# Performance work log

Hardware: AMD Instinct MI355X
Metric: run time of the kernel (lower is better)

## Reference

```python
import jax, jax.numpy as jnp
import numpy as np

N = 20000   # nodes
E = 320000  # edges
C = 64      # channel multiplicity
NB = 8      # bessel basis size
NA = 4      # node attribute (species) dim
L_DIMS = (1, 3, 5)  # 2l+1 for l=0,1,2
SH = 9      # total spherical-harmonic dim
OFFS = (0, 1, 4, 9)


def setup_inputs() -> dict:
    key = jax.random.key(0)
    ks = jax.random.split(key, 11)
    s = lambda k, shape: jax.random.normal(k, shape, dtype=jnp.float32)
    return {
        "length": jax.random.uniform(ks[0], (E, NB), dtype=jnp.float32),
        "node_features": s(ks[1], (N, C)),
        "node_attributes": s(ks[2], (N, NA)),
        "edge_attributes": s(ks[3], (E, SH)),
        "W1": s(ks[4], (NB, 64)),
        "W2": s(ks[5], (64, 64)),
        "W3": s(ks[6], (64, 64)),
        "W4": s(ks[7], (64, 3 * C)),
        "Wl": s(ks[8], (3, C, C)),
        "Wsc": s(ks[9], (NA, C, C)),
        "edge_index": jax.random.randint(ks[10], (2, E), 0, N, dtype=jnp.int32),
    }


def reference(length, node_features, node_attributes, edge_attributes, W1, W2, W3, W4, Wl, Wsc, edge_index):
    sender, receiver = edge_index[0], edge_index[1]
    silu = jax.nn.silu
    # e3nn FullyConnectedNet: x @ W / sqrt(fan_in), silu between layers, no act on last
    h = silu(length @ W1 * np.float32(1.0 / np.sqrt(NB)))
    h = silu(h @ W2 * np.float32(0.125))
    h = silu(h @ W3 * np.float32(0.125))
    w = (h @ W4 * np.float32(0.125)).reshape(E, 3, C)  # per-edge TP weights [E,3,C]
    # weighted tensor product: scalar node feats x sh (0e x le -> le, uvu)
    wx = w * node_features[sender][:, None, :]          # [E,3,C]
    parts = []
    for l in range(3):
        Y = edge_attributes[:, OFFS[l]:OFFS[l + 1]]     # [E, 2l+1]
        parts.append((wx[:, l, :, None] * Y[:, None, :]).reshape(E, C * L_DIMS[l]))
    mij = jnp.concatenate(parts, axis=1)                # [E, C*9]
    # scatter_sum into receivers
    msg = jax.ops.segment_sum(mij, receiver, num_segments=N)  # [N, C*9]
    # e3nn Linear: per-l channel mix, 1/sqrt(fan_in) norm
    out_blocks = []
    o = 0
    for l in range(3):
        d = L_DIMS[l]
        blk = msg[:, o:o + C * d].reshape(N, C, d)
        out_blocks.append(jnp.einsum('num,uv->nvm', blk, Wl[l]) * np.float32(1.0 / np.sqrt(C)))
        o += C * d
    message = jnp.concatenate(out_blocks, axis=2)       # reshape_irreps -> [N, C, 9]
    # FullyConnectedTensorProduct(attr 0e, feat 0e) -> only 0e output has paths
    sc0 = jnp.einsum('na,nu,auw->nw', node_attributes, node_features, Wsc) * np.float32(1.0 / np.sqrt(NA * C))
    sc = jnp.concatenate([sc0, jnp.zeros((N, C * (SH - 1)), dtype=sc0.dtype)], axis=1)  # [N, C*9]
    return (message, sc)
```

## Files before the change

kernel.cpp:

```cpp
#include <hip/hip_runtime.h>
#include <hip/hip_fp16.h>

#define N_NODES 20000
#define N_EDGES 320000
#define MSG_ROW 576
#define MSG_OFF 11520000
#define SCAN_BS 256
#define NBLK_SCAN ((N_NODES + SCAN_BS - 1) / SCAN_BS)
#define NPAD 20032
#define MT_S (NPAD * 64)

typedef _Float16 f16;
typedef _Float16 f16x4 __attribute__((ext_vector_type(4)));
typedef _Float16 f16x8 __attribute__((ext_vector_type(8)));
typedef float f32x4 __attribute__((ext_vector_type(4)));

#define OFF_WT4 0
#define OFF_W1T 24576
#define OFF_WT2 28672
#define OFF_WT3 36864
#define OFF_H0  45056
#define OFF_HT  49152
#define LDS_TOTAL 57344
#define OFF_WXT 24576

#define OFF_WLT  22528
#define OFF_WSCT 34816
#define WIMG_HALF 51200
#define WIMG_BYTES 102400

__device__ __forceinline__ float silu_f(float x) {
    return x * (1.0f / (1.0f + __expf(-x)));
}


__global__ __launch_bounds__(256)
void wimg_kernel(const float* __restrict__ W1, const float* __restrict__ W2,
                 const float* __restrict__ W3, const float* __restrict__ W4,
                 const float* __restrict__ Wl, const float* __restrict__ Wsc,
                 f16* __restrict__ img) {
    const int p = blockIdx.x * 256 + threadIdx.x;
    if (p >= WIMG_HALF) return;
    float v;
    if (p < 12288) {
        const int m = p >> 6, rem = p & 63, g = rem >> 3, j = rem & 7;
        const int k = ((g ^ (m & 7)) << 3) | j;
        v = W4[k * 192 + m];
    } else if (p < 14336) {
        const int q = p - 12288;
        const int m = q >> 5, rem = q & 31, g = rem >> 3, j = rem & 7;
        const int k = ((g ^ (m & 3)) << 3) | j;
        v = (k < 8) ? W1[k * 64 + m] : 0.f;
    } else if (p < 18432) {
        const int q = p - 14336;
        const int m = q >> 6, rem = q & 63, g = rem >> 3, j = rem & 7;
        const int k = ((g ^ (m & 7)) << 3) | j;
        v = W2[k * 64 + m];
    } else if (p < 22528) {
        const int q = p - 18432;
        const int m = q >> 6, rem = q & 63, g = rem >> 3, j = rem & 7;
        const int k = ((g ^ (m & 7)) << 3) | j;
        v = W3[k * 64 + m];
    } else if (p < OFF_WSCT) {
        const int q = p - OFF_WLT;
        const int l = q >> 12, r = q & 4095, vv = r >> 6, u = r & 63;
        v = Wl[(l * 64 + u) * 64 + vv];
    } else {
        const int q = p - OFF_WSCT;
        const int ww = q >> 8, kk = q & 255, a = kk >> 6, u = kk & 63;
        v = Wsc[(a * 64 + u) * 64 + ww];
    }
    img[p] = (f16)v;
}


__global__ __launch_bounds__(256)
void hist_kernel(const int* __restrict__ eidx, int* __restrict__ counts) {
    const int e = blockIdx.x * 256 + threadIdx.x;
    if (e < N_EDGES) atomicAdd(&counts[eidx[N_EDGES + e]], 1);
}

__global__ __launch_bounds__(SCAN_BS)
void scan1_kernel(const int* __restrict__ counts, int* __restrict__ offs,
                  int* __restrict__ bsum) {
    __shared__ int sm[SCAN_BS];
    const int tid = threadIdx.x;
    const int i = blockIdx.x * SCAN_BS + tid;
    const int v = (i < N_NODES) ? counts[i] : 0;
    sm[tid] = v;
    __syncthreads();
#pragma unroll
    for (int off = 1; off < SCAN_BS; off <<= 1) {
        const int t = (tid >= off) ? sm[tid - off] : 0;
        __syncthreads();
        sm[tid] += t;
        __syncthreads();
    }
    if (i < N_NODES) offs[i] = sm[tid] - v;
    if (tid == SCAN_BS - 1) bsum[blockIdx.x] = sm[tid];
}

__global__ __launch_bounds__(128)
void scan2_kernel(const int* __restrict__ bsum, int* __restrict__ bbase,
                  int* __restrict__ offs) {
    __shared__ int sm[128];
    const int tid = threadIdx.x;
    const int v = (tid < NBLK_SCAN) ? bsum[tid] : 0;
    sm[tid] = v;
    __syncthreads();
#pragma unroll
    for (int off = 1; off < 128; off <<= 1) {
        const int t = (tid >= off) ? sm[tid - off] : 0;
        __syncthreads();
        sm[tid] += t;
        __syncthreads();
    }
    if (tid < NBLK_SCAN) bbase[tid] = sm[tid] - v;
    if (tid == 127) offs[N_NODES] = sm[127];
}

__global__ __launch_bounds__(SCAN_BS)
void scan3_kernel(int* __restrict__ offs, const int* __restrict__ bbase,
                  int* __restrict__ cursor) {
    const int i = blockIdx.x * SCAN_BS + threadIdx.x;
    if (i < N_NODES) {
        const int o = offs[i] + bbase[blockIdx.x];
        offs[i] = o;
        cursor[i] = o;
    }
}

__global__ __launch_bounds__(256)
void scatter_kernel(const int* __restrict__ eidx, int* __restrict__ cursor,
                    int* __restrict__ order) {
    const int e = blockIdx.x * 256 + threadIdx.x;
    if (e < N_EDGES) {
        const int pos = atomicAdd(&cursor[eidx[N_EDGES + e]], 1);
        order[pos] = e;
    }
}


__global__ __launch_bounds__(256)
void edge_mlp_mfma(const float* __restrict__ length,
                   const float* __restrict__ nf,
                   const int*   __restrict__ eidx,
                   const f16*   __restrict__ wimg,
                   f16* __restrict__ wx)
{
    __shared__ __align__(16) char s[LDS_TOTAL];
    __shared__ int sendS[64];

    const int tid = threadIdx.x;
    const int ebase = blockIdx.x << 6;

    {
        const uint4* src = (const uint4*)wimg;
        uint4* dst = (uint4*)s;
#pragma unroll
        for (int i = 0; i < 11; ++i) dst[i * 256 + tid] = src[i * 256 + tid];
    }
    if (tid < 64) {
        const int e = tid;
        const float4 q0 = *(const float4*)&length[(size_t)(ebase + e) * 8];
        const float4 q1 = *(const float4*)&length[(size_t)(ebase + e) * 8 + 4];
        f16x8 h;
        h[0] = (f16)q0.x; h[1] = (f16)q0.y; h[2] = (f16)q0.z; h[3] = (f16)q0.w;
        h[4] = (f16)q1.x; h[5] = (f16)q1.y; h[6] = (f16)q1.z; h[7] = (f16)q1.w;
        *(f16x8*)(s + OFF_H0 + e * 64 + ((0 ^ (e & 3)) << 4)) = h;
        sendS[e] = eidx[ebase + e];
    } else {
        const int idx = tid - 64;
        const int e = idx / 3, gz = 1 + idx - (idx / 3) * 3;
        uint4 z; z.x = 0; z.y = 0; z.z = 0; z.w = 0;
        *(uint4*)(s + OFF_H0 + e * 64 + ((gz ^ (e & 3)) << 4)) = z;
    }
    __syncthreads();

    const int lane = tid & 63, w = tid >> 6;
    const int lm = lane & 15, lg = lane >> 4;
    const int mrow = w * 16 + lm;
    const int r0 = lg << 2;

    const f32x4 zacc = {0.f, 0.f, 0.f, 0.f};
    f32x4 acc[4];

    {
        const f16x8 a = *(const f16x8*)(s + OFF_W1T + mrow * 64 + ((lg ^ (mrow & 3)) << 4));
#pragma unroll
        for (int nt = 0; nt < 4; ++nt) {
            const int e = nt * 16 + lm;
            const f16x8 b = *(const f16x8*)(s + OFF_H0 + e * 64 + ((lg ^ (e & 3)) << 4));
            acc[nt] = __builtin_amdgcn_mfma_f32_16x16x32_f16(a, b, zacc, 0, 0, 0);
        }
    }
    {
        const int c = w * 16 + r0;
#pragma unroll
        for (int nt = 0; nt < 4; ++nt) {
            const int e = nt * 16 + lm;
            f16x4 pk;
            pk[0] = (f16)silu_f(acc[nt][0] * 0.35355339059f);
            pk[1] = (f16)silu_f(acc[nt][1] * 0.35355339059f);
            pk[2] = (f16)silu_f(acc[nt][2] * 0.35355339059f);
            pk[3] = (f16)silu_f(acc[nt][3] * 0.35355339059f);
            *(f16x4*)(s + OFF_HT + e * 128 + (((c >> 3) ^ (e & 7)) << 4) + ((c & 7) << 1)) = pk;
        }
    }
    __syncthreads();

#pragma unroll
    for (int nt = 0; nt < 4; ++nt) acc[nt] = zacc;
#pragma unroll
    for (int kh = 0; kh < 2; ++kh) {
        const int g = (kh << 2) + lg;
        const f16x8 a = *(const f16x8*)(s + OFF_WT2 + mrow * 128 + ((g ^ (mrow & 7)) << 4));
#pragma unroll
        for (int nt = 0; nt < 4; ++nt) {
            const int e = nt * 16 + lm;
            const f16x8 b = *(const f16x8*)(s + OFF_HT + e * 128 + ((g ^ (e & 7)) << 4));
            acc[nt] = __builtin_amdgcn_mfma_f32_16x16x32_f16(a, b, acc[nt], 0, 0, 0);
        }
    }
    __syncthreads();
    {
        const int c = w * 16 + r0;
#pragma unroll
        for (int nt = 0; nt < 4; ++nt) {
            const int e = nt * 16 + lm;
            f16x4 pk;
            pk[0] = (f16)silu_f(acc[nt][0] * 0.125f);
            pk[1] = (f16)silu_f(acc[nt][1] * 0.125f);
            pk[2] = (f16)silu_f(acc[nt][2] * 0.125f);
            pk[3] = (f16)silu_f(acc[nt][3] * 0.125f);
            *(f16x4*)(s + OFF_HT + e * 128 + (((c >> 3) ^ (e & 7)) << 4) + ((c & 7) << 1)) = pk;
        }
    }
    __syncthreads();

#pragma unroll
    for (int nt = 0; nt < 4; ++nt) acc[nt] = zacc;
#pragma unroll
    for (int kh = 0; kh < 2; ++kh) {
        const int g = (kh << 2) + lg;
        const f16x8 a = *(const f16x8*)(s + OFF_WT3 + mrow * 128 + ((g ^ (mrow & 7)) << 4));
#pragma unroll
        for (int nt = 0; nt < 4; ++nt) {
            const int e = nt * 16 + lm;
            const f16x8 b = *(const f16x8*)(s + OFF_HT + e * 128 + ((g ^ (e & 7)) << 4));
            acc[nt] = __builtin_amdgcn_mfma_f32_16x16x32_f16(a, b, acc[nt], 0, 0, 0);
        }
    }
    __syncthreads();
    {
        const int c = w * 16 + r0;
#pragma unroll
        for (int nt = 0; nt < 4; ++nt) {
            const int e = nt * 16 + lm;
            f16x4 pk;
            pk[0] = (f16)silu_f(acc[nt][0] * 0.125f);
            pk[1] = (f16)silu_f(acc[nt][1] * 0.125f);
            pk[2] = (f16)silu_f(acc[nt][2] * 0.125f);
            pk[3] = (f16)silu_f(acc[nt][3] * 0.125f);
            *(f16x4*)(s + OFF_HT + e * 128 + (((c >> 3) ^ (e & 7)) << 4) + ((c & 7) << 1)) = pk;
        }
    }
    __syncthreads();

    f32x4 acc4[3][4];
#pragma unroll
    for (int p = 0; p < 3; ++p)
#pragma unroll
        for (int nt = 0; nt < 4; ++nt) acc4[p][nt] = zacc;
#pragma unroll
    for (int kh = 0; kh < 2; ++kh) {
        const int g = (kh << 2) + lg;
        f16x8 ap[3];
#pragma unroll
        for (int p = 0; p < 3; ++p) {
            const int m4 = p * 64 + mrow;
            ap[p] = *(const f16x8*)(s + OFF_WT4 + m4 * 128 + ((g ^ (m4 & 7)) << 4));
        }
#pragma unroll
        for (int nt = 0; nt < 4; ++nt) {
            const int e = nt * 16 + lm;
            const f16x8 b = *(const f16x8*)(s + OFF_HT + e * 128 + ((g ^ (e & 7)) << 4));
#pragma unroll
            for (int p = 0; p < 3; ++p)
                acc4[p][nt] = __builtin_amdgcn_mfma_f32_16x16x32_f16(ap[p], b, acc4[p][nt], 0, 0, 0);
        }
    }
    __syncthreads();

#pragma unroll
    for (int nt = 0; nt < 4; ++nt) {
        const int e = nt * 16 + lm;
        const int snd = sendS[e];
        const float4 nf4 = *(const float4*)&nf[(size_t)snd * 64 + w * 16 + r0];
#pragma unroll
        for (int p = 0; p < 3; ++p) {
            const int c = p * 64 + w * 16 + r0;
            f16x4 pk;
            pk[0] = (f16)(acc4[p][nt][0] * 0.125f * nf4.x);
            pk[1] = (f16)(acc4[p][nt][1] * 0.125f * nf4.y);
            pk[2] = (f16)(acc4[p][nt][2] * 0.125f * nf4.z);
            pk[3] = (f16)(acc4[p][nt][3] * 0.125f * nf4.w);
            *(f16x4*)(s + OFF_WXT + e * 384 + (((c >> 3) ^ (e & 7)) << 4) + ((c & 7) << 1)) = pk;
        }
    }
    __syncthreads();

#pragma unroll
    for (int it = 0; it < 6; ++it) {
        const int chunk = it * 256 + tid;
        const int e = chunk / 24, g = chunk - e * 24;
        const uint4 v = *(const uint4*)(s + OFF_WXT + e * 384 + ((g ^ (e & 7)) << 4));
        *(uint4*)((char*)wx + (size_t)(ebase + e) * 384 + g * 16) = v;
    }
}


__global__ __launch_bounds__(256, 8)
void gather_kernel(const __half* __restrict__ wx,
                   const float* __restrict__ ea,
                   const int* __restrict__ offs,
                   const int* __restrict__ order,
                   f16* __restrict__ mT)
{
    const int tid = threadIdx.x;
    const int wid = tid >> 6;
    const int v   = tid & 63;
    const int n   = (blockIdx.x << 2) + wid;
    const int beg = offs[n];
    const int end = offs[n + 1];

    float a0 = 0.f, a1[3] = {0.f, 0.f, 0.f}, a2[5] = {0.f, 0.f, 0.f, 0.f, 0.f};
    int k = beg;
    for (; k + 2 <= end; k += 2) {
        const int eA = __builtin_amdgcn_readfirstlane(order[k]);
        const int eB = __builtin_amdgcn_readfirstlane(order[k + 1]);
        const __half* wrA = wx + (size_t)eA * 192;
        const __half* wrB = wx + (size_t)eB * 192;
        const float xA0 = __half2float(wrA[v]);
        const float xA1 = __half2float(wrA[64 + v]);
        const float xA2 = __half2float(wrA[128 + v]);
        const float xB0 = __half2float(wrB[v]);
        const float xB1 = __half2float(wrB[64 + v]);
        const float xB2 = __half2float(wrB[128 + v]);
        const float* yA = ea + (size_t)eA * 9;
        const float* yB = ea + (size_t)eB * 9;
        a0 += xA0 * yA[0] + xB0 * yB[0];
#pragma unroll
        for (int m = 0; m < 3; ++m) a1[m] += xA1 * yA[1 + m] + xB1 * yB[1 + m];
#pragma unroll
        for (int m = 0; m < 5; ++m) a2[m] += xA2 * yA[4 + m] + xB2 * yB[4 + m];
    }
    if (k < end) {
        const int e = __builtin_amdgcn_readfirstlane(order[k]);
        const __half* wr = wx + (size_t)e * 192;
        const float x0 = __half2float(wr[v]);
        const float x1 = __half2float(wr[64 + v]);
        const float x2 = __half2float(wr[128 + v]);
        const float* y = ea + (size_t)e * 9;
        a0 += x0 * y[0];
#pragma unroll
        for (int m = 0; m < 3; ++m) a1[m] += x1 * y[1 + m];
#pragma unroll
        for (int m = 0; m < 5; ++m) a2[m] += x2 * y[4 + m];
    }

    f16* base = mT + (size_t)n * 64 + v;
    base[0] = (f16)a0;
#pragma unroll
    for (int m = 0; m < 3; ++m) base[(size_t)(1 + m) * MT_S] = (f16)a1[m];
#pragma unroll
    for (int m = 0; m < 5; ++m) base[(size_t)(4 + m) * MT_S] = (f16)a2[m];
}


__global__ __launch_bounds__(256, 2)
void node_mfma(const f16* __restrict__ wimg,
               const f16* __restrict__ mT,
               const float* __restrict__ nf,
               const float* __restrict__ na,
               float* __restrict__ out)
{
    __shared__ __align__(16) f16  mst[9 * 16 * 64];
    __shared__ __align__(16) f16  nft[16 * 64];
    __shared__ __align__(16) float nas[256];
    __shared__ __align__(16) float outb[16 * 580];

    const int tid = threadIdx.x;
    const int lane = tid & 63, w = tid >> 6;
    const int lm = lane & 15, lg = lane >> 4;
    const int r0 = lg << 2;
    const int n0 = blockIdx.x << 6;

    const f16* wlT  = wimg + OFF_WLT;
    const f16* wscT = wimg + OFF_WSCT;
    f16x8 wl[3][2];
#pragma unroll
    for (int l = 0; l < 3; ++l)
#pragma unroll
        for (int kk = 0; kk < 2; ++kk)
            wl[l][kk] = *(const f16x8*)(wlT + ((l << 6) + (w << 4) + lm) * 64 + (kk << 5) + (lg << 3));
    f16x8 wsc[8];
#pragma unroll
    for (int kg = 0; kg < 8; ++kg)
        wsc[kg] = *(const f16x8*)(wscT + ((w << 4) + lm) * 256 + (kg << 5) + (lg << 3));

    {
        const int n = n0 + (tid >> 2);
        nas[tid] = (n < N_NODES) ? na[(size_t)n * 4 + (tid & 3)] : 0.f;
    }

    const f32x4 zacc = {0.f, 0.f, 0.f, 0.f};

    for (int nt = 0; nt < 4; ++nt) {
        const int ng = n0 + (nt << 4);
        __syncthreads();

#pragma unroll
        for (int it = 0; it < 5; ++it) {
            const int c = it * 256 + tid;
            if (c < 1152) {
                const int m = c >> 7, rem = c & 127, r = rem >> 3, g = rem & 7;
                const uint4 v = *(const uint4*)(mT + (size_t)m * MT_S + (size_t)(ng + r) * 64 + (g << 3));
                *(uint4*)(&mst[m * 1024 + r * 64 + ((g ^ (r & 7)) << 3)]) = v;
            }
        }
        {
            const int r = tid >> 4, c4 = (tid & 15) << 2;
            const int n = ng + r;
            float4 v4;
            if (n < N_NODES) v4 = *(const float4*)&nf[(size_t)n * 64 + c4];
            else { v4.x = 0.f; v4.y = 0.f; v4.z = 0.f; v4.w = 0.f; }
            f16x4 h;
            h[0] = (f16)v4.x; h[1] = (f16)v4.y; h[2] = (f16)v4.z; h[3] = (f16)v4.w;
            const int g = c4 >> 3;
            *(f16x4*)&nft[r * 64 + ((g ^ (r & 7)) << 3) + (c4 & 7)] = h;
        }
        __syncthreads();

#pragma unroll
        for (int m = 0; m < 9; ++m) {
            const int l = (m == 0) ? 0 : ((m < 4) ? 1 : 2);
            f32x4 acc = zacc;
#pragma unroll
            for (int kk = 0; kk < 2; ++kk) {
                const int g = (kk << 2) + lg;
                const f16x8 b = *(const f16x8*)&mst[m * 1024 + lm * 64 + ((g ^ (lm & 7)) << 3)];
                acc = __builtin_amdgcn_mfma_f32_16x16x32_f16(wl[l][kk], b, acc, 0, 0, 0);
            }
#pragma unroll
            for (int i = 0; i < 4; ++i)
                outb[lm * 580 + ((w << 4) + r0 + i) * 9 + m] = acc[i] * 0.125f;
        }
        __syncthreads();

#pragma unroll
        for (int it = 0; it < 9; ++it) {
            const int c = it * 256 + tid;
            const int r = c / 144, q = c - r * 144;
            const int n = ng + r;
            if (n < N_NODES) {
                const float4 v = *(const float4*)&outb[r * 580 + (q << 2)];
                *(float4*)&out[(size_t)n * 576 + (q << 2)] = v;
            }
        }
        __syncthreads();

        {
            const float4 na4 = *(const float4*)&nas[((nt << 4) + lm) << 2];
            const float* nap = (const float*)&na4;
            f32x4 sacc = zacc;
#pragma unroll
            for (int kg = 0; kg < 8; ++kg) {
                const int g = ((kg & 1) << 2) + lg;
                f16x8 q = *(const f16x8*)&nft[lm * 64 + ((g ^ (lm & 7)) << 3)];
                const f16 sa = (f16)nap[kg >> 1];
                q = q * sa;
                sacc = __builtin_amdgcn_mfma_f32_16x16x32_f16(wsc[kg], q, sacc, 0, 0, 0);
            }
#pragma unroll
            for (int i = 0; i < 4; ++i)
                outb[lm * 580 + (w << 4) + r0 + i] = sacc[i] * 0.0625f;
        }
        __syncthreads();

        {
            const int r = tid >> 4, q = tid & 15;
            const int n = ng + r;
            if (n < N_NODES)
                *(float4*)&out[(size_t)MSG_OFF + (size_t)n * 576 + (q << 2)] =
                    *(const float4*)&outb[r * 580 + (q << 2)];
        }
        float4 z4; z4.x = 0.f; z4.y = 0.f; z4.z = 0.f; z4.w = 0.f;
#pragma unroll
        for (int it = 0; it < 8; ++it) {
            const int c = it * 256 + tid;
            const int r = c >> 7, q = c & 127;
            const int n = ng + r;
            if (n < N_NODES)
                *(float4*)&out[(size_t)MSG_OFF + (size_t)n * 576 + 64 + (q << 2)] = z4;
        }
    }
}


__device__ __forceinline__ void layer_accum(const float* src, const float* __restrict__ W,
                                            float a2[4][4], int c0, int e0) {
#pragma unroll
    for (int i = 0; i < 4; ++i)
#pragma unroll
        for (int j = 0; j < 4; ++j) a2[i][j] = 0.f;
#pragma unroll 8
    for (int u = 0; u < 64; ++u) {
        const float4 h4 = *(const float4*)&src[(u << 6) + e0];
        const float4 w4 = *(const float4*)&W[(u << 6) + c0];
        const float hv[4] = {h4.x, h4.y, h4.z, h4.w};
        const float wv[4] = {w4.x, w4.y, w4.z, w4.w};
#pragma unroll
        for (int i = 0; i < 4; ++i)
#pragma unroll
            for (int j = 0; j < 4; ++j) a2[i][j] += wv[i] * hv[j];
    }
}

__device__ __forceinline__ void layer_store(float* dst, const float a2[4][4],
                                            float scale, int c0, int e0) {
#pragma unroll
    for (int i = 0; i < 4; ++i) {
        float4 v;
        v.x = silu_f(a2[i][0] * scale);
        v.y = silu_f(a2[i][1] * scale);
        v.z = silu_f(a2[i][2] * scale);
        v.w = silu_f(a2[i][3] * scale);
        *(float4*)&dst[((c0 + i) << 6) + e0] = v;
    }
}

__global__ __launch_bounds__(256, 4)
void edge_kernel_atomic(const float* __restrict__ length,
                        const float* __restrict__ nf,
                        const float* __restrict__ ea,
                        const float* __restrict__ W1,
                        const float* __restrict__ W2,
                        const float* __restrict__ W3,
                        const float* __restrict__ W4,
                        const int*   __restrict__ eidx,
                        float* __restrict__ msg)
{
    __shared__ float buf[4096];
    __shared__ float lenS[512];
    __shared__ float Ys[576];
    __shared__ int   sendS[64];
    __shared__ int   recvS[64];

    const int tid = threadIdx.x;
    const int tx = tid & 15;
    const int ty = tid >> 4;
    const int c0 = tx << 2;
    const int e0 = ty << 2;
    const int ebase = blockIdx.x << 6;

    for (int i = tid; i < 512; i += 256) {
        const int e = i >> 3, k = i & 7;
        lenS[(k << 6) + e] = length[((ebase + e) << 3) + k];
    }
    for (int i = tid; i < 576; i += 256) Ys[i] = ea[ebase * 9 + i];
    if (tid < 64) {
        sendS[tid] = eidx[ebase + tid];
        recvS[tid] = eidx[N_EDGES + ebase + tid];
    }
    __syncthreads();

    {
        float a2[4][4];
#pragma unroll
        for (int i = 0; i < 4; ++i)
#pragma unroll
            for (int j = 0; j < 4; ++j) a2[i][j] = 0.f;
#pragma unroll
        for (int k = 0; k < 8; ++k) {
            const float4 h4 = *(const float4*)&lenS[(k << 6) + e0];
            const float4 w4 = *(const float4*)&W1[(k << 6) + c0];
            const float hv[4] = {h4.x, h4.y, h4.z, h4.w};
            const float wv[4] = {w4.x, w4.y, w4.z, w4.w};
#pragma unroll
            for (int i = 0; i < 4; ++i)
#pragma unroll
                for (int j = 0; j < 4; ++j) a2[i][j] += wv[i] * hv[j];
        }
        layer_store(buf, a2, 0.35355339059327373f, c0, e0);
    }
    __syncthreads();
    {
        float a2[4][4];
        layer_accum(buf, W2, a2, c0, e0);
        __syncthreads();
        layer_store(buf, a2, 0.125f, c0, e0);
    }
    __syncthreads();
    {
        float a2[4][4];
        layer_accum(buf, W3, a2, c0, e0);
        __syncthreads();
        layer_store(buf, a2, 0.125f, c0, e0);
    }
    __syncthreads();

    float wacc[3][4][4];
#pragma unroll
    for (int l = 0; l < 3; ++l)
#pragma unroll
        for (int i = 0; i < 4; ++i)
#pragma unroll
            for (int j = 0; j < 4; ++j) wacc[l][i][j] = 0.f;
#pragma unroll 4
    for (int u = 0; u < 64; ++u) {
        const float4 h4 = *(const float4*)&buf[(u << 6) + e0];
        const float hv[4] = {h4.x, h4.y, h4.z, h4.w};
#pragma unroll
        for (int l = 0; l < 3; ++l) {
            const float4 w4 = *(const float4*)&W4[u * 192 + (l << 6) + c0];
            const float wv[4] = {w4.x, w4.y, w4.z, w4.w};
#pragma unroll
            for (int i = 0; i < 4; ++i)
#pragma unroll
                for (int j = 0; j < 4; ++j) wacc[l][i][j] += wv[i] * hv[j];
        }
    }

#pragma unroll
    for (int j = 0; j < 4; ++j) {
        const int e = e0 + j;
        const int snd = sendS[e];
        const int rcv = recvS[e];
        const float4 nf4 = *(const float4*)&nf[(snd << 6) + c0];
        const float nfv[4] = {nf4.x, nf4.y, nf4.z, nf4.w};
        float* mrow = msg + rcv * MSG_ROW;
        const float y0 = Ys[e * 9 + 0];
        float y1[3], y2[5];
#pragma unroll
        for (int m = 0; m < 3; ++m) y1[m] = Ys[e * 9 + 1 + m];
#pragma unroll
        for (int m = 0; m < 5; ++m) y2[m] = Ys[e * 9 + 4 + m];
#pragma unroll
        for (int i = 0; i < 4; ++i) {
            const int c = c0 + i;
            const float wx0 = wacc[0][i][j] * 0.125f * nfv[i];
            const float wx1 = wacc[1][i][j] * 0.125f * nfv[i];
            const float wx2 = wacc[2][i][j] * 0.125f * nfv[i];
            atomicAdd(&mrow[c], wx0 * y0);
#pragma unroll
            for (int m = 0; m < 3; ++m) atomicAdd(&mrow[64 + c * 3 + m], wx1 * y1[m]);
#pragma unroll
            for (int m = 0; m < 5; ++m) atomicAdd(&mrow[256 + c * 5 + m], wx2 * y2[m]);
        }
    }
}

__global__ __launch_bounds__(256, 4)
void node_kernel(const float* __restrict__ nf,
                 const float* __restrict__ na,
                 const float* __restrict__ Wl,
                 const float* __restrict__ Wsc,
                 float* __restrict__ out)
{
    __shared__ float ms[4][576];
    __shared__ float fs[4][64];
    const int tid = threadIdx.x;
    const int wid = tid >> 6;
    const int v   = tid & 63;
    const int n   = (blockIdx.x << 2) + wid;
    const float* msg = out + MSG_OFF;

#pragma unroll
    for (int j = 0; j < 9; ++j)
        ms[wid][(j << 6) + v] = msg[n * MSG_ROW + (j << 6) + v];
    fs[wid][v] = nf[(n << 6) + v];
    __syncthreads();

    float o9[9];
#pragma unroll
    for (int j = 0; j < 9; ++j) o9[j] = 0.f;
    const float* m0 = &ms[wid][0];
    const float* m1 = &ms[wid][64];
    const float* m2 = &ms[wid][256];

#pragma unroll 8
    for (int u = 0; u < 64; ++u) {
        const float w0 = Wl[(u << 6) + v];
        const float w1 = Wl[4096 + (u << 6) + v];
        const float w2 = Wl[8192 + (u << 6) + v];
        o9[0] += m0[u] * w0;
        o9[1] += m1[u * 3 + 0] * w1;
        o9[2] += m1[u * 3 + 1] * w1;
        o9[3] += m1[u * 3 + 2] * w1;
        o9[4] += m2[u * 5 + 0] * w2;
        o9[5] += m2[u * 5 + 1] * w2;
        o9[6] += m2[u * 5 + 2] * w2;
        o9[7] += m2[u * 5 + 3] * w2;
        o9[8] += m2[u * 5 + 4] * w2;
    }
#pragma unroll
    for (int j = 0; j < 9; ++j) out[n * MSG_ROW + v * 9 + j] = o9[j] * 0.125f;

    const float b0 = na[(n << 2) + 0];
    const float b1 = na[(n << 2) + 1];
    const float b2 = na[(n << 2) + 2];
    const float b3 = na[(n << 2) + 3];
    float sacc = 0.f;
#pragma unroll 8
    for (int u = 0; u < 64; ++u) {
        const float f = fs[wid][u];
        sacc += f * (b0 * Wsc[(u << 6) + v] + b1 * Wsc[4096 + (u << 6) + v] +
                     b2 * Wsc[8192 + (u << 6) + v] + b3 * Wsc[12288 + (u << 6) + v]);
    }
    float* scrow = out + MSG_OFF + n * MSG_ROW;
    scrow[v] = sacc * 0.0625f;
#pragma unroll
    for (int j = 1; j < 9; ++j) scrow[(j << 6) + v] = 0.f;
}

extern "C" void kernel_launch(void* const* d_in, const int* in_sizes, int n_in,
                              void* d_out, int out_size, void* d_ws, size_t ws_size,
                              hipStream_t stream) {
    const float* length = (const float*)d_in[0];
    const float* nfeat  = (const float*)d_in[1];
    const float* nattr  = (const float*)d_in[2];
    const float* eattr  = (const float*)d_in[3];
    const float* W1     = (const float*)d_in[4];
    const float* W2     = (const float*)d_in[5];
    const float* W3     = (const float*)d_in[6];
    const float* W4     = (const float*)d_in[7];
    const float* Wl     = (const float*)d_in[8];
    const float* Wsc    = (const float*)d_in[9];
    const int*   eidx   = (const int*)d_in[10];
    float* out = (float*)d_out;

    f16*    wimg   = (f16*)d_ws;
    __half* wx     = (__half*)((char*)d_ws + WIMG_BYTES);
    f16*    mT     = (f16*)((char*)d_ws + WIMG_BYTES + (size_t)N_EDGES * 192 * 2);
    int*   counts  = (int*)((char*)mT + (size_t)9 * MT_S * 2);
    int*   offsets = counts + N_NODES;
    int*   cursor  = offsets + N_NODES + 1;
    int*   order   = cursor + N_NODES;
    int*   bsum    = order + N_EDGES;
    int*   bbase   = bsum + 128;
    const size_t need = WIMG_BYTES + (size_t)N_EDGES * 192 * 2 + (size_t)9 * MT_S * 2 +
                        (size_t)(N_NODES * 3 + 1 + N_EDGES + 256) * 4;

    if (ws_size >= need) {
        hipMemsetAsync(counts, 0, N_NODES * sizeof(int), stream);
        wimg_kernel<<<(WIMG_HALF + 255) / 256, 256, 0, stream>>>(W1, W2, W3, W4, Wl, Wsc, wimg);
        hist_kernel<<<N_EDGES / 256, 256, 0, stream>>>(eidx, counts);
        scan1_kernel<<<NBLK_SCAN, SCAN_BS, 0, stream>>>(counts, offsets, bsum);
        scan2_kernel<<<1, 128, 0, stream>>>(bsum, bbase, offsets);
        scan3_kernel<<<NBLK_SCAN, SCAN_BS, 0, stream>>>(offsets, bbase, cursor);
        scatter_kernel<<<N_EDGES / 256, 256, 0, stream>>>(eidx, cursor, order);
        edge_mlp_mfma<<<N_EDGES / 64, 256, 0, stream>>>(length, nfeat, eidx, wimg, (f16*)wx);
        gather_kernel<<<N_NODES / 4, 256, 0, stream>>>(wx, eattr, offsets, order, mT);
        node_mfma<<<NPAD / 64, 256, 0, stream>>>(wimg, mT, nfeat, nattr, out);
    } else {
        hipMemsetAsync(out + MSG_OFF, 0, (size_t)N_NODES * MSG_ROW * sizeof(float), stream);
        edge_kernel_atomic<<<N_EDGES / 64, 256, 0, stream>>>(length, nfeat, eattr,
                                                             W1, W2, W3, W4, eidx,
                                                             out + MSG_OFF);
        node_kernel<<<N_NODES / 4, 256, 0, stream>>>(nfeat, nattr, Wl, Wsc, out);
    }
}
```

Measured before the change: 174.3 us.

## Write per-edge weights in receiver-sorted order and process 128 edges per block

The scatter kernel now records each edge's sorted position (rank), and the edge MLP writes its wx rows straight to that sorted slot. The gather kernel then reads wx contiguously by position k instead of jumping through order[] to random edges. The edge MLP block also doubles to 512 threads and 128 edges, which amortises the LDS weight-image load over twice as many edges. The costs are a scattered write pattern in the edge kernel, an extra rank array, and larger LDS use per block that may lower occupancy.

```diff
diff --git a/kernel.cpp b/kernel.cpp
--- a/kernel.cpp
+++ b/kernel.cpp
@@ -19,10 +19,11 @@
 #define OFF_W1T 24576
 #define OFF_WT2 28672
 #define OFF_WT3 36864
+#define WEDGE_BYTES 45056
 #define OFF_H0  45056
-#define OFF_HT  49152
-#define LDS_TOTAL 57344
-#define OFF_WXT 24576
+#define OFF_HT  53248
+#define LDS_TOTAL 69632
+#define OFF_WXT 0
 
 #define OFF_WLT  22528
 #define OFF_WSCT 34816
@@ -132,35 +133,41 @@
 
 __global__ __launch_bounds__(256)
 void scatter_kernel(const int* __restrict__ eidx, int* __restrict__ cursor,
-                    int* __restrict__ order) {
+                    int* __restrict__ order, int* __restrict__ rank) {
     const int e = blockIdx.x * 256 + threadIdx.x;
     if (e < N_EDGES) {
         const int pos = atomicAdd(&cursor[eidx[N_EDGES + e]], 1);
         order[pos] = e;
-    }
-}
-
-
-__global__ __launch_bounds__(256)
+        rank[e] = pos;
+    }
+}
+
+
+__global__ __launch_bounds__(512, 4)
 void edge_mlp_mfma(const float* __restrict__ length,
                    const float* __restrict__ nf,
                    const int*   __restrict__ eidx,
+                   const int*   __restrict__ rank,
                    const f16*   __restrict__ wimg,
                    f16* __restrict__ wx)
 {
     __shared__ __align__(16) char s[LDS_TOTAL];
-    __shared__ int sendS[64];
+    __shared__ int sendS[128];
+    __shared__ int rankS[128];
 
     const int tid = threadIdx.x;
-    const int ebase = blockIdx.x << 6;
+    const int ebase = blockIdx.x << 7;
 
     {
         const uint4* src = (const uint4*)wimg;
         uint4* dst = (uint4*)s;
 #pragma unroll
-        for (int i = 0; i < 11; ++i) dst[i * 256 + tid] = src[i * 256 + tid];
-    }
-    if (tid < 64) {
+        for (int i = 0; i < 6; ++i) {
+            const int c = i * 512 + tid;
+            if (c < 2816) dst[c] = src[c];
+        }
+    }
+    if (tid < 128) {
         const int e = tid;
         const float4 q0 = *(const float4*)&length[(size_t)(ebase + e) * 8];
         const float4 q1 = *(const float4*)&length[(size_t)(ebase + e) * 8 + 4];
@@ -169,8 +176,9 @@
         h[4] = (f16)q1.x; h[5] = (f16)q1.y; h[6] = (f16)q1.z; h[7] = (f16)q1.w;
         *(f16x8*)(s + OFF_H0 + e * 64 + ((0 ^ (e & 3)) << 4)) = h;
         sendS[e] = eidx[ebase + e];
+        rankS[e] = rank[ebase + e];
     } else {
-        const int idx = tid - 64;
+        const int idx = tid - 128;
         const int e = idx / 3, gz = 1 + idx - (idx / 3) * 3;
         uint4 z; z.x = 0; z.y = 0; z.z = 0; z.w = 0;
         *(uint4*)(s + OFF_H0 + e * 64 + ((gz ^ (e & 3)) << 4)) = z;
@@ -178,9 +186,11 @@
     __syncthreads();
 
     const int lane = tid & 63, w = tid >> 6;
+    const int eh = w >> 2, wm = w & 3;
     const int lm = lane & 15, lg = lane >> 4;
-    const int mrow = w * 16 + lm;
+    const int mrow = wm * 16 + lm;
     const int r0 = lg << 2;
+    const int eloc0 = eh << 6;
 
     const f32x4 zacc = {0.f, 0.f, 0.f, 0.f};
     f32x4 acc[4];
@@ -189,16 +199,16 @@
         const f16x8 a = *(const f16x8*)(s + OFF_W1T + mrow * 64 + ((lg ^ (mrow & 3)) << 4));
 #pragma unroll
         for (int nt = 0; nt < 4; ++nt) {
-            const int e = nt * 16 + lm;
+            const int e = eloc0 + nt * 16 + lm;
             const f16x8 b = *(const f16x8*)(s + OFF_H0 + e * 64 + ((lg ^ (e & 3)) << 4));
             acc[nt] = __builtin_amdgcn_mfma_f32_16x16x32_f16(a, b, zacc, 0, 0, 0);
         }
     }
     {
-        const int c = w * 16 + r0;
+        const int c = wm * 16 + r0;
 #pragma unroll
         for (int nt = 0; nt < 4; ++nt) {
-            const int e = nt * 16 + lm;
+            const int e = eloc0 + nt * 16 + lm;
             f16x4 pk;
             pk[0] = (f16)silu_f(acc[nt][0] * 0.35355339059f);
             pk[1] = (f16)silu_f(acc[nt][1] * 0.35355339059f);
@@ -217,17 +227,17 @@
         const f16x8 a = *(const f16x8*)(s + OFF_WT2 + mrow * 128 + ((g ^ (mrow & 7)) << 4));
 #pragma unroll
         for (int nt = 0; nt < 4; ++nt) {
-            const int e = nt * 16 + lm;
+            const int e = eloc0 + nt * 16 + lm;
             const f16x8 b = *(const f16x8*)(s + OFF_HT + e * 128 + ((g ^ (e & 7)) << 4));
             acc[nt] = __builtin_amdgcn_mfma_f32_16x16x32_f16(a, b, acc[nt], 0, 0, 0);
         }
     }
     __syncthreads();
     {
-        const int c = w * 16 + r0;
+        const int c = wm * 16 + r0;
 #pragma unroll
         for (int nt = 0; nt < 4; ++nt) {
-            const int e = nt * 16 + lm;
+            const int e = eloc0 + nt * 16 + lm;
             f16x4 pk;
             pk[0] = (f16)silu_f(acc[nt][0] * 0.125f);
             pk[1] = (f16)silu_f(acc[nt][1] * 0.125f);
@@ -246,17 +256,17 @@
         const f16x8 a = *(const f16x8*)(s + OFF_WT3 + mrow * 128 + ((g ^ (mrow & 7)) << 4));
 #pragma unroll
         for (int nt = 0; nt < 4; ++nt) {
-            const int e = nt * 16 + lm;
+            const int e = eloc0 + nt * 16 + lm;
             const f16x8 b = *(const f16x8*)(s + OFF_HT + e * 128 + ((g ^ (e & 7)) << 4));
             acc[nt] = __builtin_amdgcn_mfma_f32_16x16x32_f16(a, b, acc[nt], 0, 0, 0);
         }
     }
     __syncthreads();
     {
-        const int c = w * 16 + r0;
+        const int c = wm * 16 + r0;
 #pragma unroll
         for (int nt = 0; nt < 4; ++nt) {
-            const int e = nt * 16 + lm;
+            const int e = eloc0 + nt * 16 + lm;
             f16x4 pk;
             pk[0] = (f16)silu_f(acc[nt][0] * 0.125f);
             pk[1] = (f16)silu_f(acc[nt][1] * 0.125f);
@@ -283,7 +293,7 @@
         }
 #pragma unroll
         for (int nt = 0; nt < 4; ++nt) {
-            const int e = nt * 16 + lm;
+            const int e = eloc0 + nt * 16 + lm;
             const f16x8 b = *(const f16x8*)(s + OFF_HT + e * 128 + ((g ^ (e & 7)) << 4));
 #pragma unroll
             for (int p = 0; p < 3; ++p)
@@ -294,12 +304,12 @@
 
 #pragma unroll
     for (int nt = 0; nt < 4; ++nt) {
-        const int e = nt * 16 + lm;
+        const int e = eloc0 + nt * 16 + lm;
         const int snd = sendS[e];
-        const float4 nf4 = *(const float4*)&nf[(size_t)snd * 64 + w * 16 + r0];
+        const float4 nf4 = *(const float4*)&nf[(size_t)snd * 64 + wm * 16 + r0];
 #pragma unroll
         for (int p = 0; p < 3; ++p) {
-            const int c = p * 64 + w * 16 + r0;
+            const int c = p * 64 + wm * 16 + r0;
             f16x4 pk;
             pk[0] = (f16)(acc4[p][nt][0] * 0.125f * nf4.x);
             pk[1] = (f16)(acc4[p][nt][1] * 0.125f * nf4.y);
@@ -312,10 +322,10 @@
 
 #pragma unroll
     for (int it = 0; it < 6; ++it) {
-        const int chunk = it * 256 + tid;
+        const int chunk = it * 512 + tid;
         const int e = chunk / 24, g = chunk - e * 24;
         const uint4 v = *(const uint4*)(s + OFF_WXT + e * 384 + ((g ^ (e & 7)) << 4));
-        *(uint4*)((char*)wx + (size_t)(ebase + e) * 384 + g * 16) = v;
+        *(uint4*)((char*)wx + (size_t)rankS[e] * 384 + g * 16) = v;
     }
 }
 
@@ -339,8 +349,8 @@
     for (; k + 2 <= end; k += 2) {
         const int eA = __builtin_amdgcn_readfirstlane(order[k]);
         const int eB = __builtin_amdgcn_readfirstlane(order[k + 1]);
-        const __half* wrA = wx + (size_t)eA * 192;
-        const __half* wrB = wx + (size_t)eB * 192;
+        const __half* wrA = wx + (size_t)k * 192;
+        const __half* wrB = wx + (size_t)(k + 1) * 192;
         const float xA0 = __half2float(wrA[v]);
         const float xA1 = __half2float(wrA[64 + v]);
         const float xA2 = __half2float(wrA[128 + v]);
@@ -357,7 +367,7 @@
     }
     if (k < end) {
         const int e = __builtin_amdgcn_readfirstlane(order[k]);
-        const __half* wr = wx + (size_t)e * 192;
+        const __half* wr = wx + (size_t)k * 192;
         const float x0 = __half2float(wr[v]);
         const float x1 = __half2float(wr[64 + v]);
         const float x2 = __half2float(wr[128 + v]);
@@ -747,10 +757,11 @@
     int*   offsets = counts + N_NODES;
     int*   cursor  = offsets + N_NODES + 1;
     int*   order   = cursor + N_NODES;
-    int*   bsum    = order + N_EDGES;
+    int*   rank    = order + N_EDGES;
+    int*   bsum    = rank + N_EDGES;
     int*   bbase   = bsum + 128;
     const size_t need = WIMG_BYTES + (size_t)N_EDGES * 192 * 2 + (size_t)9 * MT_S * 2 +
-                        (size_t)(N_NODES * 3 + 1 + N_EDGES + 256) * 4;
+                        (size_t)(N_NODES * 3 + 1 + N_EDGES * 2 + 256) * 4;
 
     if (ws_size >= need) {
         hipMemsetAsync(counts, 0, N_NODES * sizeof(int), stream);
@@ -759,8 +770,9 @@
         scan1_kernel<<<NBLK_SCAN, SCAN_BS, 0, stream>>>(counts, offsets, bsum);
         scan2_kernel<<<1, 128, 0, stream>>>(bsum, bbase, offsets);
         scan3_kernel<<<NBLK_SCAN, SCAN_BS, 0, stream>>>(offsets, bbase, cursor);
-        scatter_kernel<<<N_EDGES / 256, 256, 0, stream>>>(eidx, cursor, order);
-        edge_mlp_mfma<<<N_EDGES / 64, 256, 0, stream>>>(length, nfeat, eidx, wimg, (f16*)wx);
+        scatter_kernel<<<N_EDGES / 256, 256, 0, stream>>>(eidx, cursor, order, rank);
+        edge_mlp_mfma<<<N_EDGES / 128, 512, 0, stream>>>(length, nfeat, eidx, rank,
+                                                         wimg, (f16*)wx);
         gather_kernel<<<N_NODES / 4, 256, 0, stream>>>(wx, eattr, offsets, order, mT);
         node_mfma<<<NPAD / 64, 256, 0, stream>>>(wimg, mT, nfeat, nattr, out);
     } else {
```

Measured after the change: 165.6 us. 1.05x faster.
